# Optimization experiments

Measured on AMD Instinct MI355X. Metric: run time of the kernel, lower is better.

Reference implementation:

```python
import jax, jax.numpy as jnp
import numpy as np

B = 262144          # batch of sample points
L = 16              # hash levels
T = 1 << 19         # hash table size per level
F = 2               # features per level
BASE_RES = 16
FINEST_RES = 512
DH = 64             # density MLP hidden
DOUT = 16           # density MLP out (density_out dim)
CH = 64             # color MLP hidden
PRIMES = np.array([1, 2654435761, 805459861], dtype=np.uint32)
_b = np.exp((np.log(FINEST_RES) - np.log(BASE_RES)) / (L - 1))
RES = jnp.asarray(np.floor(BASE_RES * _b ** np.arange(L)).astype(np.float32))  # (L,)


def _linear_init(key, fan_in, fan_out):
    kw, kb = jax.random.split(key)
    bound = 1.0 / np.sqrt(fan_in)
    w = jax.random.uniform(kw, (fan_in, fan_out), minval=-bound, maxval=bound)
    b = jax.random.uniform(kb, (fan_out,), minval=-bound, maxval=bound)
    return w, b


def setup_inputs() -> dict:
    key = jax.random.key(0)
    ks = jax.random.split(key, 10)
    coords = jax.random.uniform(ks[0], (B, 3), dtype=jnp.float32)          # in [0,1]
    directions = jax.random.normal(ks[1], (B, 3), dtype=jnp.float32)
    embeddings = jax.random.uniform(ks[2], (L, T, F), minval=-1e-4, maxval=1e-4, dtype=jnp.float32)
    dw1, db1 = _linear_init(ks[3], L * F, DH)
    dw2, db2 = _linear_init(ks[4], DH, DOUT)
    cw1, cb1 = _linear_init(ks[5], 16 + DOUT, CH)
    cw2, cb2 = _linear_init(ks[6], CH, CH)
    cw3, cb3 = _linear_init(ks[7], CH, CH)
    cw4, cb4 = _linear_init(ks[8], CH, 3)
    return dict(coords=coords, directions=directions, embeddings=embeddings,
                dw1=dw1, db1=db1, dw2=dw2, db2=db2,
                cw1=cw1, cb1=cb1, cw2=cw2, cb2=cb2,
                cw3=cw3, cb3=cb3, cw4=cw4, cb4=cb4)


def hash_encode(coords, embeddings):
    # coords: (B,3) in [0,1]; embeddings: (L,T,F)
    pos = coords[:, None, :] * RES[None, :, None]            # (B,L,3)
    p0 = jnp.floor(pos)
    frac = pos - p0                                           # (B,L,3)
    p0 = p0.astype(jnp.uint32)
    corners = jnp.stack([p0, p0 + jnp.uint32(1)], axis=-1)    # (B,L,3,2)
    h_ax = corners * jnp.asarray(PRIMES)[None, None, :, None]  # uint32 wraparound
    hidx = (h_ax[:, :, 0, :, None, None]
            ^ h_ax[:, :, 1, None, :, None]
            ^ h_ax[:, :, 2, None, None, :])                   # (B,L,2,2,2)
    hidx = (hidx & jnp.uint32(T - 1)).reshape(coords.shape[0], L, 8).astype(jnp.int32)
    feats = embeddings[jnp.arange(L)[None, :, None], hidx]    # (B,L,8,F)
    wx = jnp.stack([1.0 - frac[..., 0], frac[..., 0]], -1)    # (B,L,2)
    wy = jnp.stack([1.0 - frac[..., 1], frac[..., 1]], -1)
    wz = jnp.stack([1.0 - frac[..., 2], frac[..., 2]], -1)
    w = (wx[:, :, :, None, None] * wy[:, :, None, :, None] * wz[:, :, None, None, :])
    w = w.reshape(coords.shape[0], L, 8)                      # (B,L,8)
    out = jnp.sum(feats * w[..., None], axis=2)               # (B,L,F)
    return out.reshape(coords.shape[0], L * F)


def sh_encode_deg4(d):
    # d: (B,3) unit directions in [-1,1]; degree-4 real SH basis (16 comps)
    x, y, z = d[:, 0], d[:, 1], d[:, 2]
    xx, yy, zz = x * x, y * y, z * z
    xy, yz, xz = x * y, y * z, x * z
    c = jnp.full_like(x, 0.28209479177387814)
    return jnp.stack([
        c,
        -0.48860251190291987 * y,
        0.48860251190291987 * z,
        -0.48860251190291987 * x,
        1.0925484305920792 * xy,
        -1.0925484305920792 * yz,
        0.94617469575755997 * zz - 0.31539156525251999,
        -1.0925484305920792 * xz,
        0.54627421529603959 * (xx - yy),
        0.59004358992664352 * y * (-3.0 * xx + yy),
        2.8906114426405538 * xy * z,
        0.45704579946446572 * y * (1.0 - 5.0 * zz),
        0.3731763325901154 * z * (5.0 * zz - 3.0),
        0.45704579946446572 * x * (1.0 - 5.0 * zz),
        1.4453057213202769 * z * (xx - yy),
        0.59004358992664352 * x * (xx - 3.0 * yy),
    ], axis=1)


def reference(coords, directions, embeddings, dw1, db1, dw2, db2,
              cw1, cb1, cw2, cb2, cw3, cb3, cw4, cb4):
    # density net: hash encode -> Linear+ReLU -> Linear
    feat = hash_encode(coords, embeddings)                    # (B, L*F)
    h = jax.nn.relu(feat @ dw1 + db1)
    density_out = h @ dw2 + db2                               # (B, DOUT)
    density = jnp.exp(density_out[:, 0])                      # TruncExp fwd = exp
    # color net
    d = directions / jnp.linalg.norm(directions, axis=1, keepdims=True)
    d01 = (d + 1.0) / 2.0                                     # remap as in module
    sh = sh_encode_deg4(d01 * 2.0 - 1.0)                      # encoder maps back to [-1,1]
    inp = jnp.concatenate([sh, density_out], axis=1)          # (B, 32)
    x = jax.nn.relu(inp @ cw1 + cb1)
    x = jax.nn.relu(x @ cw2 + cb2)
    x = jax.nn.relu(x @ cw3 + cb3)
    color = jax.nn.sigmoid(x @ cw4 + cb4)                     # (B, 3)
    return density, color
```

## Files before the change

### kernel.cpp

```cpp
#include <hip/hip_runtime.h>
#include <cmath>

#define NPTS 262144
#define NLVL 16
#define TBL  524288u
#define TMASK 524287u
#define TPB  128
#define NQ   6

typedef __attribute__((ext_vector_type(8))) short short8;
typedef __attribute__((ext_vector_type(4))) float f32x4;

struct ResArr { float r[NLVL]; };
struct QuadInfo { int off[NQ]; int dim[NQ]; };

__device__ __forceinline__ unsigned short f2bf(float f) {
    union { float f; unsigned u; } v; v.f = f;
    unsigned r = v.u + 0x7FFFu + ((v.u >> 16) & 1u);
    return (unsigned short)(r >> 16);
}
__device__ __forceinline__ float blo(unsigned u) {
    union { unsigned v; float f; } x; x.v = u << 16; return x.f;
}
__device__ __forceinline__ float bhi(unsigned u) {
    union { unsigned v; float f; } x; x.v = u & 0xffff0000u; return x.f;
}

#define MFMA(a,b,c) __builtin_amdgcn_mfma_f32_16x16x32_bf16((a),(b),(c),0,0,0)

__global__ __launch_bounds__(256) void densify_quad_k(
    const float* __restrict__ emb,
    uint4* __restrict__ quad,
    QuadInfo qi)
{
    const int l = blockIdx.y;
    const int t = blockIdx.x * 256 + threadIdx.x;
    const int D = qi.dim[l];
    if (t >= D*D*D) return;
    const unsigned z = (unsigned)t % (unsigned)D;
    const unsigned rem = (unsigned)t / (unsigned)D;
    const unsigned y = rem % (unsigned)D;
    const unsigned x = rem / (unsigned)D;

    const float2* __restrict__ emb2 = (const float2*)emb;
    const unsigned base = (unsigned)l * TBL;
    const unsigned hy0 = y*2654435761u, hy1 = (y+1u)*2654435761u;
    const unsigned hz0 = z*805459861u,  hz1 = (z+1u)*805459861u;

    const float2 a = emb2[base + ((x^hy0^hz0)&TMASK)];
    const float2 b = emb2[base + ((x^hy0^hz1)&TMASK)];
    const float2 c = emb2[base + ((x^hy1^hz0)&TMASK)];
    const float2 d = emb2[base + ((x^hy1^hz1)&TMASK)];

    uint4 q;
    q.x = (unsigned)f2bf(a.x) | ((unsigned)f2bf(a.y) << 16);
    q.y = (unsigned)f2bf(b.x) | ((unsigned)f2bf(b.y) << 16);
    q.z = (unsigned)f2bf(c.x) | ((unsigned)f2bf(c.y) << 16);
    q.w = (unsigned)f2bf(d.x) | ((unsigned)f2bf(d.y) << 16);
    quad[qi.off[l] + t] = q;
}

__global__ __launch_bounds__(256) void hash_encode_k(
    const float* __restrict__ coords,
    const float* __restrict__ emb,
    const uint4* __restrict__ quad,
    unsigned* __restrict__ featws,
    ResArr res, QuadInfo qi)
{
    const int tid = threadIdx.x;
    const int b   = blockIdx.x;
    const int xcd = b & 7;
    const int s   = b >> 3;

    if (s < 1024 || xcd >= 3) {
        int l, p;
        if (s < 1024) {
            l = 6 + xcd;
            p = s * 256 + tid;
        } else {
            if (xcd == 7) return;
            const int u  = (s - 1024) >> 8;
            const int c  = (s - 1024) & 255;
            const int gq = (xcd - 3) * 2 + u;
            l = (gq < 4) ? 14 : 15;
            p = ((gq & 3) * 256 + c) * 256 + tid;
        }

        const float cx = coords[3*p], cy = coords[3*p+1], cz = coords[3*p+2];
        const float r = res.r[l];
        const float px = cx*r, py = cy*r, pz = cz*r;
        const float fpx = floorf(px), fpy = floorf(py), fpz = floorf(pz);
        const float fx = px-fpx, fy = py-fpy, fz = pz-fpz;
        const unsigned ix=(unsigned)fpx, iy=(unsigned)fpy, iz=(unsigned)fpz;
        const unsigned hx0=ix,             hx1=ix+1u;
        const unsigned hy0=iy*2654435761u, hy1=(iy+1u)*2654435761u;
        const unsigned hz0=iz*805459861u,  hz1=(iz+1u)*805459861u;
        const unsigned base = (unsigned)l * TBL;
        const float2* __restrict__ emb2 = (const float2*)emb;

        const float2 f000 = emb2[base + ((hx0^hy0^hz0)&TMASK)];
        const float2 f001 = emb2[base + ((hx0^hy0^hz1)&TMASK)];
        const float2 f010 = emb2[base + ((hx0^hy1^hz0)&TMASK)];
        const float2 f011 = emb2[base + ((hx0^hy1^hz1)&TMASK)];
        const float2 f100 = emb2[base + ((hx1^hy0^hz0)&TMASK)];
        const float2 f101 = emb2[base + ((hx1^hy0^hz1)&TMASK)];
        const float2 f110 = emb2[base + ((hx1^hy1^hz0)&TMASK)];
        const float2 f111 = emb2[base + ((hx1^hy1^hz1)&TMASK)];

        const float wx0=1.f-fx, wy0=1.f-fy, wz0=1.f-fz;
        float o0, o1;
        o0 = wx0*wy0*wz0*f000.x;                 o1 = wx0*wy0*wz0*f000.y;
        o0 = fmaf(wx0*wy0*fz,  f001.x, o0);      o1 = fmaf(wx0*wy0*fz,  f001.y, o1);
        o0 = fmaf(wx0*fy*wz0,  f010.x, o0);      o1 = fmaf(wx0*fy*wz0,  f010.y, o1);
        o0 = fmaf(wx0*fy*fz,   f011.x, o0);      o1 = fmaf(wx0*fy*fz,   f011.y, o1);
        o0 = fmaf(fx*wy0*wz0,  f100.x, o0);      o1 = fmaf(fx*wy0*wz0,  f100.y, o1);
        o0 = fmaf(fx*wy0*fz,   f101.x, o0);      o1 = fmaf(fx*wy0*fz,   f101.y, o1);
        o0 = fmaf(fx*fy*wz0,   f110.x, o0);      o1 = fmaf(fx*fy*wz0,   f110.y, o1);
        o0 = fmaf(fx*fy*fz,    f111.x, o0);      o1 = fmaf(fx*fy*fz,    f111.y, o1);

        featws[(size_t)l * NPTS + p] = (unsigned)f2bf(o0) | ((unsigned)f2bf(o1) << 16);
    } else {
        const int u  = (s - 1024) >> 8;
        const int c  = (s - 1024) & 255;
        const int l  = 2*xcd + u;
        const int D  = qi.dim[l];
        const int DD = D*D;
        const int off = qi.off[l];
        const float r = res.r[l];

        int   pidx[4];
        uint4 qA[4], qB[4];
        float fxa[4], fya[4], fza[4];
        #pragma unroll
        for (int k = 0; k < 4; ++k) {
            const int p = c*1024 + k*256 + tid;
            pidx[k] = p;
            const float cx = coords[3*p], cy = coords[3*p+1], cz = coords[3*p+2];
            const float px = cx*r, py = cy*r, pz = cz*r;
            const float fpx = floorf(px), fpy = floorf(py), fpz = floorf(pz);
            fxa[k] = px-fpx; fya[k] = py-fpy; fza[k] = pz-fpz;
            const int ix=(int)fpx, iy=(int)fpy, iz=(int)fpz;
            const int v0 = off + (ix*D + iy)*D + iz;
            qA[k] = quad[v0];
            qB[k] = quad[v0 + DD];
        }
        #pragma unroll
        for (int k = 0; k < 4; ++k) {
            const float fx = fxa[k], fy = fya[k], fz = fza[k];
            const float wx0=1.f-fx, wy0=1.f-fy, wz0=1.f-fz;
            const float w000=wx0*wy0*wz0, w001=wx0*wy0*fz;
            const float w010=wx0*fy*wz0,  w011=wx0*fy*fz;
            const float w100=fx*wy0*wz0,  w101=fx*wy0*fz;
            const float w110=fx*fy*wz0,   w111=fx*fy*fz;
            float o0, o1;
            o0 = w000*blo(qA[k].x);              o1 = w000*bhi(qA[k].x);
            o0 = fmaf(w001, blo(qA[k].y), o0);   o1 = fmaf(w001, bhi(qA[k].y), o1);
            o0 = fmaf(w010, blo(qA[k].z), o0);   o1 = fmaf(w010, bhi(qA[k].z), o1);
            o0 = fmaf(w011, blo(qA[k].w), o0);   o1 = fmaf(w011, bhi(qA[k].w), o1);
            o0 = fmaf(w100, blo(qB[k].x), o0);   o1 = fmaf(w100, bhi(qB[k].x), o1);
            o0 = fmaf(w101, blo(qB[k].y), o0);   o1 = fmaf(w101, bhi(qB[k].y), o1);
            o0 = fmaf(w110, blo(qB[k].z), o0);   o1 = fmaf(w110, bhi(qB[k].z), o1);
            o0 = fmaf(w111, blo(qB[k].w), o0);   o1 = fmaf(w111, bhi(qB[k].w), o1);
            featws[(size_t)l * NPTS + pidx[k]] =
                (unsigned)f2bf(o0) | ((unsigned)f2bf(o1) << 16);
        }
    }
}

__global__ __launch_bounds__(256, 3) void mlp_mfma_k(
    const unsigned* __restrict__ featws,
    const float* __restrict__ dirs,
    const float* __restrict__ dw1, const float* __restrict__ db1,
    const float* __restrict__ dw2, const float* __restrict__ db2,
    const float* __restrict__ cw1, const float* __restrict__ cb1,
    const float* __restrict__ cw2, const float* __restrict__ cb2,
    const float* __restrict__ cw3, const float* __restrict__ cb3,
    const float* __restrict__ cw4, const float* __restrict__ cb4,
    float* __restrict__ out)
{
    const int tid  = threadIdx.x;
    const int wid  = tid >> 6;
    const int lane = tid & 63;
    const int m16  = lane & 15;
    const int q    = lane >> 4;

    __shared__ __align__(16) unsigned short wlds[28 * 512];
    __shared__ float blds[288];
    __shared__ __align__(16) unsigned short featL[TPB * 40];
    __shared__ __align__(16) unsigned short actL[4 * 16 * 72];

    const unsigned char MAT[28] = {0,0,0,0, 1,1, 2,2,2,2, 3,3,3,3,3,3,3,3, 4,4,4,4,4,4,4,4, 5,5};
    const unsigned char K0 [28] = {0,0,0,0, 0,32, 0,0,0,0, 0,0,0,0,32,32,32,32, 0,0,0,0,32,32,32,32, 0,32};
    const unsigned char N0 [28] = {0,16,32,48, 0,0, 0,16,32,48, 0,16,32,48,0,16,32,48, 0,16,32,48,0,16,32,48, 0,0};

    #pragma unroll
    for (int s = 0; s < 28; ++s) {
        if ((s & 3) == wid) {
            const int mat = MAT[s];
            const float* src = mat==0?dw1 : mat==1?dw2 : mat==2?cw1 : mat==3?cw2 : mat==4?cw3 : cw4;
            const int fan = (mat==1) ? 16 : (mat==5) ? 3 : 64;
            const int k = (int)K0[s] + q*8;
            const int n = (int)N0[s] + m16;
            unsigned short u[8];
            #pragma unroll
            for (int j = 0; j < 8; ++j) {
                float v = 0.f;
                if (mat != 5 || n < 3) v = src[(k+j)*fan + n];
                u[j] = f2bf(v);
            }
            unsigned* w32 = (unsigned*)(wlds + s*512 + lane*8);
            w32[0] = (unsigned)u[0] | ((unsigned)u[1] << 16);
            w32[1] = (unsigned)u[2] | ((unsigned)u[3] << 16);
            w32[2] = (unsigned)u[4] | ((unsigned)u[5] << 16);
            w32[3] = (unsigned)u[6] | ((unsigned)u[7] << 16);
        }
    }
    {
        int t = tid;
        if      (t <  64) blds[t] = db1[t];
        else if (t <  80) blds[t] = db2[t-64];
        else if (t < 144) blds[t] = cb1[t-80];
        else if (t < 208) blds[t] = cb2[t-144];
    }
    if (tid < 80) {
        int t = tid + 208;
        if (t < 272) blds[t] = cb3[t-208];
        else         blds[t] = (t-272 < 3) ? cb4[t-272] : 0.f;
    }

    const int pbase = blockIdx.x * TPB;
    unsigned* fL32 = (unsigned*)featL;
    #pragma unroll
    for (int j = 0; j < 8; ++j) {
        const int idx  = j*256 + tid;
        const int l    = idx >> 7;
        const int ploc = idx & 127;
        fL32[ploc*20 + l] = featws[(size_t)l * NPTS + pbase + ploc];
    }
    __syncthreads();

    unsigned short* aw = actL + wid*1152;
    const short8* wfr = (const short8*)wlds;

    #pragma unroll
    for (int iter = 0; iter < 2; ++iter) {
        const int tile = wid + 4*iter;
        const int loc0 = tile*16;
        const int p0g  = pbase + loc0;

        short8 a0 = *(const short8*)(featL + (loc0+m16)*40 + q*8);
        f32x4 acc[4];
        #pragma unroll
        for (int nc = 0; nc < 4; ++nc) {
            const float b = blds[nc*16 + m16];
            acc[nc] = (f32x4){b,b,b,b};
            acc[nc] = MFMA(a0, wfr[nc*64 + lane], acc[nc]);
        }
        #pragma unroll
        for (int nc = 0; nc < 4; ++nc)
            #pragma unroll
            for (int r = 0; r < 4; ++r)
                aw[(q*4+r)*72 + nc*16 + m16] = f2bf(fmaxf(acc[nc][r], 0.f));

        short8 ad0 = *(const short8*)(aw + m16*72 + q*8);
        short8 ad1 = *(const short8*)(aw + m16*72 + 32 + q*8);
        f32x4 dob;
        { const float b = blds[64 + m16]; dob = (f32x4){b,b,b,b}; }
        dob = MFMA(ad0, wfr[4*64 + lane], dob);
        dob = MFMA(ad1, wfr[5*64 + lane], dob);

        if (m16 == 0) {
            #pragma unroll
            for (int r = 0; r < 4; ++r) out[p0g + q*4 + r] = expf(dob[r]);
        }

        #pragma unroll
        for (int r = 0; r < 4; ++r)
            aw[(q*4+r)*72 + 16 + m16] = f2bf(dob[r]);
        {
            const int pg = p0g + m16;
            const float dx0 = dirs[3*pg], dy0 = dirs[3*pg+1], dz0 = dirs[3*pg+2];
            const float inv = 1.f / sqrtf(dx0*dx0 + dy0*dy0 + dz0*dz0);
            float x = dx0*inv, y = dy0*inv, z = dz0*inv;
            x = ((x+1.f)*0.5f)*2.f - 1.f;
            y = ((y+1.f)*0.5f)*2.f - 1.f;
            z = ((z+1.f)*0.5f)*2.f - 1.f;
            float s0, s1, s2, s3;
            switch (q) {
            case 0: s0 = 0.28209479177387814f;
                    s1 = -0.48860251190291987f*y;
                    s2 =  0.48860251190291987f*z;
                    s3 = -0.48860251190291987f*x; break;
            case 1: s0 =  1.0925484305920792f*x*y;
                    s1 = -1.0925484305920792f*y*z;
                    s2 =  0.94617469575756f*z*z - 0.31539156525252f;
                    s3 = -1.0925484305920792f*x*z; break;
            case 2: s0 =  0.5462742152960396f*(x*x - y*y);
                    s1 =  0.5900435899266435f*y*(-3.f*x*x + y*y);
                    s2 =  2.890611442640554f*x*y*z;
                    s3 =  0.4570457994644657f*y*(1.f - 5.f*z*z); break;
            default:s0 =  0.3731763325901154f*z*(5.f*z*z - 3.f);
                    s1 =  0.4570457994644657f*x*(1.f - 5.f*z*z);
                    s2 =  1.445305721320277f*z*(x*x - y*y);
                    s3 =  0.5900435899266435f*x*(x*x - 3.f*y*y); break;
            }
            unsigned* ip = (unsigned*)(aw + m16*72 + q*4);
            ip[0] = (unsigned)f2bf(s0) | ((unsigned)f2bf(s1) << 16);
            ip[1] = (unsigned)f2bf(s2) | ((unsigned)f2bf(s3) << 16);
        }

        short8 ac0 = *(const short8*)(aw + m16*72 + q*8);
        #pragma unroll
        for (int nc = 0; nc < 4; ++nc) {
            const float b = blds[80 + nc*16 + m16];
            acc[nc] = (f32x4){b,b,b,b};
            acc[nc] = MFMA(ac0, wfr[(6+nc)*64 + lane], acc[nc]);
        }
        #pragma unroll
        for (int nc = 0; nc < 4; ++nc)
            #pragma unroll
            for (int r = 0; r < 4; ++r)
                aw[(q*4+r)*72 + nc*16 + m16] = f2bf(fmaxf(acc[nc][r], 0.f));

        short8 a20 = *(const short8*)(aw + m16*72 + q*8);
        short8 a21 = *(const short8*)(aw + m16*72 + 32 + q*8);
        #pragma unroll
        for (int nc = 0; nc < 4; ++nc) {
            const float b = blds[144 + nc*16 + m16];
            acc[nc] = (f32x4){b,b,b,b};
            acc[nc] = MFMA(a20, wfr[(10+nc)*64 + lane], acc[nc]);
            acc[nc] = MFMA(a21, wfr[(14+nc)*64 + lane], acc[nc]);
        }
        #pragma unroll
        for (int nc = 0; nc < 4; ++nc)
            #pragma unroll
            for (int r = 0; r < 4; ++r)
                aw[(q*4+r)*72 + nc*16 + m16] = f2bf(fmaxf(acc[nc][r], 0.f));

        short8 a30 = *(const short8*)(aw + m16*72 + q*8);
        short8 a31 = *(const short8*)(aw + m16*72 + 32 + q*8);
        #pragma unroll
        for (int nc = 0; nc < 4; ++nc) {
            const float b = blds[208 + nc*16 + m16];
            acc[nc] = (f32x4){b,b,b,b};
            acc[nc] = MFMA(a30, wfr[(18+nc)*64 + lane], acc[nc]);
            acc[nc] = MFMA(a31, wfr[(22+nc)*64 + lane], acc[nc]);
        }
        #pragma unroll
        for (int nc = 0; nc < 4; ++nc)
            #pragma unroll
            for (int r = 0; r < 4; ++r)
                aw[(q*4+r)*72 + nc*16 + m16] = f2bf(fmaxf(acc[nc][r], 0.f));

        short8 a40 = *(const short8*)(aw + m16*72 + q*8);
        short8 a41 = *(const short8*)(aw + m16*72 + 32 + q*8);
        f32x4 c4;
        { const float b = blds[272 + m16]; c4 = (f32x4){b,b,b,b}; }
        c4 = MFMA(a40, wfr[26*64 + lane], c4);
        c4 = MFMA(a41, wfr[27*64 + lane], c4);
        if (m16 < 3) {
            #pragma unroll
            for (int r = 0; r < 4; ++r)
                out[NPTS + 3*(p0g + q*4 + r) + m16] = 1.f / (1.f + expf(-c4[r]));
        }
    }
}

extern "C" void kernel_launch(void* const* d_in, const int* in_sizes, int n_in,
                              void* d_out, int out_size, void* d_ws, size_t ws_size,
                              hipStream_t stream)
{
    ResArr res;
    const double b = exp((log(512.0) - log(16.0)) / 15.0);
    for (int l = 0; l < NLVL; ++l)
        res.r[l] = (float)floor(16.0 * pow(b, (double)l));

    QuadInfo qi;
    int off = 0, maxn = 0;
    for (int l = 0; l < NQ; ++l) {
        const int D = (int)res.r[l] + 1;
        qi.dim[l] = D;
        qi.off[l] = off;
        off += D*D*D;
        if (D*D*D > maxn) maxn = D*D*D;
    }

    unsigned* featws = (unsigned*)d_ws;
    uint4*    quad   = (uint4*)((char*)d_ws + (size_t)NLVL * NPTS * 4);

    densify_quad_k<<<dim3((maxn + 255)/256, NQ), 256, 0, stream>>>(
        (const float*)d_in[2], quad, qi);

    hash_encode_k<<<12288, 256, 0, stream>>>(
        (const float*)d_in[0],
        (const float*)d_in[2],
        quad, featws, res, qi);

    mlp_mfma_k<<<NPTS/TPB, 256, 0, stream>>>(
        featws,
        (const float*)d_in[1],
        (const float*)d_in[3],  (const float*)d_in[4],
        (const float*)d_in[5],  (const float*)d_in[6],
        (const float*)d_in[7],  (const float*)d_in[8],
        (const float*)d_in[9],  (const float*)d_in[10],
        (const float*)d_in[11], (const float*)d_in[12],
        (const float*)d_in[13], (const float*)d_in[14],
        (float*)d_out);
}
```

Before: 262.6 us.

## Densify level 6 into quad table and prepack MLP weights once

Level 6 now also gets a dense bf16 corner-quad table, so it reads one contiguous 16-byte pair per point instead of eight hashed float2 gathers. The hash-encode block-to-level mapping is rebalanced so that levels 7–15 use hashed lookups and levels 0–6 use quad lookups, which shrinks the grid. A separate one-block kernel converts the MLP weights to bf16 MFMA fragment layout once. Each MLP block then copies the prepacked buffer instead of redoing strided float loads and conversion. In exchange, the densify pass and workspace grow by roughly 4 MB for the larger level, and one extra tiny launch is added.

```diff
diff --git a/kernel.cpp b/kernel.cpp
--- a/kernel.cpp
+++ b/kernel.cpp
@@ -6,7 +6,7 @@
 #define TBL  524288u
 #define TMASK 524287u
 #define TPB  128
-#define NQ   6
+#define NQ   7
 
 typedef __attribute__((ext_vector_type(8))) short short8;
 typedef __attribute__((ext_vector_type(4))) float f32x4;
@@ -27,6 +27,61 @@
 }
 
 #define MFMA(a,b,c) __builtin_amdgcn_mfma_f32_16x16x32_bf16((a),(b),(c),0,0,0)
+
+__global__ __launch_bounds__(256) void wpack_k(
+    const float* __restrict__ dw1, const float* __restrict__ db1,
+    const float* __restrict__ dw2, const float* __restrict__ db2,
+    const float* __restrict__ cw1, const float* __restrict__ cb1,
+    const float* __restrict__ cw2, const float* __restrict__ cb2,
+    const float* __restrict__ cw3, const float* __restrict__ cb3,
+    const float* __restrict__ cw4, const float* __restrict__ cb4,
+    unsigned short* __restrict__ wpk, float* __restrict__ bpk)
+{
+    const int tid  = threadIdx.x;
+    const int wid  = tid >> 6;
+    const int lane = tid & 63;
+    const int m16  = lane & 15;
+    const int q    = lane >> 4;
+
+    const unsigned char MAT[28] = {0,0,0,0, 1,1, 2,2,2,2, 3,3,3,3,3,3,3,3, 4,4,4,4,4,4,4,4, 5,5};
+    const unsigned char K0 [28] = {0,0,0,0, 0,32, 0,0,0,0, 0,0,0,0,32,32,32,32, 0,0,0,0,32,32,32,32, 0,32};
+    const unsigned char N0 [28] = {0,16,32,48, 0,0, 0,16,32,48, 0,16,32,48,0,16,32,48, 0,16,32,48,0,16,32,48, 0,0};
+
+    #pragma unroll
+    for (int s = 0; s < 28; ++s) {
+        if ((s & 3) == wid) {
+            const int mat = MAT[s];
+            const float* src = mat==0?dw1 : mat==1?dw2 : mat==2?cw1 : mat==3?cw2 : mat==4?cw3 : cw4;
+            const int fan = (mat==1) ? 16 : (mat==5) ? 3 : 64;
+            const int k = (int)K0[s] + q*8;
+            const int n = (int)N0[s] + m16;
+            unsigned short u[8];
+            #pragma unroll
+            for (int j = 0; j < 8; ++j) {
+                float v = 0.f;
+                if (mat != 5 || n < 3) v = src[(k+j)*fan + n];
+                u[j] = f2bf(v);
+            }
+            unsigned* w32 = (unsigned*)(wpk + s*512 + lane*8);
+            w32[0] = (unsigned)u[0] | ((unsigned)u[1] << 16);
+            w32[1] = (unsigned)u[2] | ((unsigned)u[3] << 16);
+            w32[2] = (unsigned)u[4] | ((unsigned)u[5] << 16);
+            w32[3] = (unsigned)u[6] | ((unsigned)u[7] << 16);
+        }
+    }
+    {
+        int t = tid;
+        if      (t <  64) bpk[t] = db1[t];
+        else if (t <  80) bpk[t] = db2[t-64];
+        else if (t < 144) bpk[t] = cb1[t-80];
+        else if (t < 208) bpk[t] = cb2[t-144];
+    }
+    if (tid < 80) {
+        int t = tid + 208;
+        if (t < 272) bpk[t] = cb3[t-208];
+        else         bpk[t] = (t-272 < 3) ? cb4[t-272] : 0.f;
+    }
+}
 
 __global__ __launch_bounds__(256) void densify_quad_k(
     const float* __restrict__ emb,
@@ -72,18 +127,14 @@
     const int xcd = b & 7;
     const int s   = b >> 3;
 
-    if (s < 1024 || xcd >= 3) {
+    if (s < 1152) {
         int l, p;
         if (s < 1024) {
-            l = 6 + xcd;
+            l = 7 + xcd;
             p = s * 256 + tid;
         } else {
-            if (xcd == 7) return;
-            const int u  = (s - 1024) >> 8;
-            const int c  = (s - 1024) & 255;
-            const int gq = (xcd - 3) * 2 + u;
-            l = (gq < 4) ? 14 : 15;
-            p = ((gq & 3) * 256 + c) * 256 + tid;
+            l = 15;
+            p = xcd * 32768 + (s - 1024) * 256 + tid;
         }
 
         const float cx = coords[3*p], cy = coords[3*p+1], cz = coords[3*p+2];
@@ -120,9 +171,9 @@
 
         featws[(size_t)l * NPTS + p] = (unsigned)f2bf(o0) | ((unsigned)f2bf(o1) << 16);
     } else {
-        const int u  = (s - 1024) >> 8;
-        const int c  = (s - 1024) & 255;
-        const int l  = 2*xcd + u;
+        const int g  = xcd * 224 + (s - 1152);
+        const int l  = g >> 8;
+        const int c  = g & 255;
         const int D  = qi.dim[l];
         const int DD = D*D;
         const int off = qi.off[l];
@@ -169,13 +220,9 @@
 
 __global__ __launch_bounds__(256, 3) void mlp_mfma_k(
     const unsigned* __restrict__ featws,
+    const unsigned short* __restrict__ wpk,
+    const float* __restrict__ bpk,
     const float* __restrict__ dirs,
-    const float* __restrict__ dw1, const float* __restrict__ db1,
-    const float* __restrict__ dw2, const float* __restrict__ db2,
-    const float* __restrict__ cw1, const float* __restrict__ cb1,
-    const float* __restrict__ cw2, const float* __restrict__ cb2,
-    const float* __restrict__ cw3, const float* __restrict__ cb3,
-    const float* __restrict__ cw4, const float* __restrict__ cb4,
     float* __restrict__ out)
 {
     const int tid  = threadIdx.x;
@@ -189,43 +236,13 @@
     __shared__ __align__(16) unsigned short featL[TPB * 40];
     __shared__ __align__(16) unsigned short actL[4 * 16 * 72];
 
-    const unsigned char MAT[28] = {0,0,0,0, 1,1, 2,2,2,2, 3,3,3,3,3,3,3,3, 4,4,4,4,4,4,4,4, 5,5};
-    const unsigned char K0 [28] = {0,0,0,0, 0,32, 0,0,0,0, 0,0,0,0,32,32,32,32, 0,0,0,0,32,32,32,32, 0,32};
-    const unsigned char N0 [28] = {0,16,32,48, 0,0, 0,16,32,48, 0,16,32,48,0,16,32,48, 0,16,32,48,0,16,32,48, 0,0};
-
-    #pragma unroll
-    for (int s = 0; s < 28; ++s) {
-        if ((s & 3) == wid) {
-            const int mat = MAT[s];
-            const float* src = mat==0?dw1 : mat==1?dw2 : mat==2?cw1 : mat==3?cw2 : mat==4?cw3 : cw4;
-            const int fan = (mat==1) ? 16 : (mat==5) ? 3 : 64;
-            const int k = (int)K0[s] + q*8;
-            const int n = (int)N0[s] + m16;
-            unsigned short u[8];
-            #pragma unroll
-            for (int j = 0; j < 8; ++j) {
-                float v = 0.f;
-                if (mat != 5 || n < 3) v = src[(k+j)*fan + n];
-                u[j] = f2bf(v);
-            }
-            unsigned* w32 = (unsigned*)(wlds + s*512 + lane*8);
-            w32[0] = (unsigned)u[0] | ((unsigned)u[1] << 16);
-            w32[1] = (unsigned)u[2] | ((unsigned)u[3] << 16);
-            w32[2] = (unsigned)u[4] | ((unsigned)u[5] << 16);
-            w32[3] = (unsigned)u[6] | ((unsigned)u[7] << 16);
-        }
-    }
     {
-        int t = tid;
-        if      (t <  64) blds[t] = db1[t];
-        else if (t <  80) blds[t] = db2[t-64];
-        else if (t < 144) blds[t] = cb1[t-80];
-        else if (t < 208) blds[t] = cb2[t-144];
-    }
-    if (tid < 80) {
-        int t = tid + 208;
-        if (t < 272) blds[t] = cb3[t-208];
-        else         blds[t] = (t-272 < 3) ? cb4[t-272] : 0.f;
+        uint4* dst = (uint4*)wlds;
+        const uint4* srcv = (const uint4*)wpk;
+        #pragma unroll
+        for (int j = 0; j < 7; ++j) dst[j*256 + tid] = srcv[j*256 + tid];
+        if (tid < 288) blds[tid] = bpk[tid];
+        if (tid < 32)  blds[256 + tid] = bpk[256 + tid];
     }
 
     const int pbase = blockIdx.x * TPB;
@@ -385,25 +402,30 @@
         if (D*D*D > maxn) maxn = D*D*D;
     }
 
-    unsigned* featws = (unsigned*)d_ws;
-    uint4*    quad   = (uint4*)((char*)d_ws + (size_t)NLVL * NPTS * 4);
-
-    densify_quad_k<<<dim3((maxn + 255)/256, NQ), 256, 0, stream>>>(
-        (const float*)d_in[2], quad, qi);
-
-    hash_encode_k<<<12288, 256, 0, stream>>>(
-        (const float*)d_in[0],
-        (const float*)d_in[2],
-        quad, featws, res, qi);
-
-    mlp_mfma_k<<<NPTS/TPB, 256, 0, stream>>>(
-        featws,
-        (const float*)d_in[1],
+    unsigned*       featws = (unsigned*)d_ws;
+    uint4*          quad   = (uint4*)((char*)d_ws + (size_t)NLVL * NPTS * 4);
+    unsigned short* wpk    = (unsigned short*)((char*)quad + (size_t)off * 16);
+    float*          bpk    = (float*)((char*)wpk + 28 * 512 * 2);
+
+    wpack_k<<<1, 256, 0, stream>>>(
         (const float*)d_in[3],  (const float*)d_in[4],
         (const float*)d_in[5],  (const float*)d_in[6],
         (const float*)d_in[7],  (const float*)d_in[8],
         (const float*)d_in[9],  (const float*)d_in[10],
         (const float*)d_in[11], (const float*)d_in[12],
         (const float*)d_in[13], (const float*)d_in[14],
+        wpk, bpk);
+
+    densify_quad_k<<<dim3((maxn + 255)/256, NQ), 256, 0, stream>>>(
+        (const float*)d_in[2], quad, qi);
+
+    hash_encode_k<<<11008, 256, 0, stream>>>(
+        (const float*)d_in[0],
+        (const float*)d_in[2],
+        quad, featws, res, qi);
+
+    mlp_mfma_k<<<NPTS/TPB, 256, 0, stream>>>(
+        featws, wpk, bpk,
+        (const float*)d_in[1],
         (float*)d_out);
 }
```

Measured after the change: 254.6 us. 3.0% less time.
